# Kernel tuning notes

Hardware: AMD Instinct MI355X
Metric: run time of the kernel (lower is better)

Reference implementation:

```python
import jax, jax.numpy as jnp
import numpy as np


def setup_inputs() -> dict:
    key = jax.random.key(0)
    X = jax.random.normal(key, (8, 64, 64, 64), dtype=jnp.float32)
    return {"X": X}


def reference(X):
    N, C, h, w = X.shape
    x1 = X.reshape(N, C, h * w)            # [N, C, HW]
    x2 = jnp.transpose(x1, (0, 2, 1))      # [N, HW, C]
    scores = jnp.einsum('bnc,bcm->bnm', x2, x1)  # [N, HW, HW]
    c = jax.nn.softmax(scores, axis=2)
    out = jnp.einsum('bnm,bmc->bnc', c, x2)      # [N, HW, C]
    out = jnp.transpose(out, (0, 2, 1)).reshape(N, C, h, w)
    return out
```

## Files before the change

kernel.cpp:

```cpp
#include <hip/hip_runtime.h>
#include <math.h>


#define SEQ 4096
#define DIM 64
#define LDB 72
#define LDO 68
#define LDS2 68
#define QSCALE 1.2011224087864498f

typedef __attribute__((ext_vector_type(8)))  short short8;
typedef __attribute__((ext_vector_type(4)))  float f32x4;
typedef __attribute__((ext_vector_type(16))) float f32x16;

__device__ __forceinline__ unsigned short f2bf(float f) {
    union { float f; unsigned int u; } x; x.f = f;
    unsigned int u = x.u + 0x7FFFu + ((x.u >> 16) & 1u);
    return (unsigned short)(u >> 16);
}
__device__ __forceinline__ float bf2f(unsigned short h) {
    union { unsigned int u; float f; } x; x.u = ((unsigned int)h) << 16; return x.f;
}
__device__ __forceinline__ float fast_exp2(float x) {
#if __has_builtin(__builtin_amdgcn_exp2f)
    return __builtin_amdgcn_exp2f(x);
#else
    float r;
    asm("v_exp_f32 %0, %1\n\ts_nop 0" : "=v"(r) : "v"(x));
    return r;
#endif
}
__device__ __forceinline__ float fast_rcp(float x) {
#if __has_builtin(__builtin_amdgcn_rcpf)
    return __builtin_amdgcn_rcpf(x);
#else
    return 1.f / x;
#endif
}

__global__ __launch_bounds__(256) void prepass4(const float* __restrict__ X,
                                                unsigned short* __restrict__ Kf,
                                                unsigned short* __restrict__ Vf,
                                                float* __restrict__ Norms,
                                                float* __restrict__ MaxPart) {
    __shared__ __align__(16) unsigned short sT[64 * LDS2];
    __shared__ __align__(16) unsigned short sVu[64 * LDS2];
    __shared__ float sRed[4];
    const int b = blockIdx.y, m0 = blockIdx.x * 64;
    const float* Xb = X + (size_t)b * DIM * SEQ;
    const int t = threadIdx.x, w = t >> 6;
    const int mw = t & 15, cg = t >> 4;

    #pragma unroll
    for (int cr = 0; cr < 4; ++cr) {
        const int c = cg * 4 + cr;
        const f32x4 v = *(const f32x4*)(Xb + (size_t)c * SEQ + m0 + 4 * mw);
        *(ushort4*)(sVu + c * LDS2 + 4 * mw) =
            make_ushort4(f2bf(v.x), f2bf(v.y), f2bf(v.z), f2bf(v.w));
        sT[(4 * mw + 0) * LDS2 + c] = f2bf(v.x * QSCALE);
        sT[(4 * mw + 1) * LDS2 + c] = f2bf(v.y * QSCALE);
        sT[(4 * mw + 2) * LDS2 + c] = f2bf(v.z * QSCALE);
        sT[(4 * mw + 3) * LDS2 + c] = f2bf(v.w * QSCALE);
    }
    __syncthreads();

    {
        const int l = t & 63, ch = t >> 6;
        const int l31 = l & 31, hi = l >> 5;
        #pragma unroll
        for (int tl = 0; tl < 2; ++tl) {
            const short8 a = *(const short8*)(sT + (tl * 32 + l31) * LDS2 + ch * 16 + hi * 8);
            const size_t off = (size_t)b * 262144
                             + (size_t)(((m0 >> 5) + tl) * 4 + ch) * 512 + (size_t)l * 8;
            *(short8*)(Kf + off) = a;
        }
    }

    {
        const int m = t >> 2, ck = t & 3;
        const short8 a0 = *(const short8*)(sT + m * LDS2 + ck * 16);
        const short8 a1 = *(const short8*)(sT + m * LDS2 + ck * 16 + 8);
        float s = 0.f;
        #pragma unroll
        for (int i = 0; i < 8; ++i) {
            const float f0 = bf2f((unsigned short)a0[i]);
            const float f1 = bf2f((unsigned short)a1[i]);
            s += f0 * f0 + f1 * f1;
        }
        s += __shfl_xor(s, 1);
        s += __shfl_xor(s, 2);
        const float nm = sqrtf(s);
        if (ck == 0) Norms[(size_t)b * SEQ + m0 + m] = nm;

        float mx = nm;
        #pragma unroll
        for (int d = 4; d < 64; d <<= 1) mx = fmaxf(mx, __shfl_xor(mx, d));
        if ((t & 63) == 0) sRed[w] = mx;
    }

    {
        const int l = t & 63, pc = t >> 6;
        const int p = pc >> 1, ct = pc & 1;
        const int l31 = l & 31, hi = l >> 5;
        const int crow = (ct * 32 + l31) * LDS2;
        #pragma unroll
        for (int tl = 0; tl < 2; ++tl) {
            const int kbase = tl * 32 + p * 16 + hi * 4;
            const ushort4 g0 = *(const ushort4*)(sVu + crow + kbase);
            const ushort4 g1 = *(const ushort4*)(sVu + crow + kbase + 8);
            union { ushort4 g[2]; short8 v; } cat;
            cat.g[0] = g0; cat.g[1] = g1;
            const size_t off = (size_t)b * 262144
                             + (size_t)(((m0 >> 5) + tl) * 4 + p * 2 + ct) * 512 + (size_t)l * 8;
            *(short8*)(Vf + off) = cat.v;
        }
    }

    __syncthreads();
    if (t == 0)
        MaxPart[b * 64 + blockIdx.x] =
            fmaxf(fmaxf(sRed[0], sRed[1]), fmaxf(sRed[2], sRed[3]));
}

#if __has_builtin(__builtin_amdgcn_global_load_lds)
#define STAGE(BI, SOFF)                                                            \
    {                                                                              \
        unsigned short* dst_ = ring + (BI) * 4096 + (w ? 2048 : 0);                \
        const unsigned short* src_ = (w ? vgp : kgp) + (SOFF);                     \
        _Pragma("unroll")                                                          \
        for (int j_ = 0; j_ < 4; ++j_)                                             \
            __builtin_amdgcn_global_load_lds(                                      \
                (const __attribute__((address_space(1))) unsigned int*)(const void*)(src_ + j_ * 512), \
                (__attribute__((address_space(3))) unsigned int*)(void*)(dst_ + j_ * 512),             \
                16, 0, 0);                                                         \
    }
#else
#define STAGE(BI, SOFF)                                                            \
    {                                                                              \
        unsigned short* dst_ = ring + (BI) * 4096 + (w ? 2048 : 0) + lane * 8;     \
        const unsigned short* src_ = (w ? vgp : kgp) + (SOFF);                     \
        _Pragma("unroll")                                                          \
        for (int j_ = 0; j_ < 4; ++j_)                                             \
            *(short8*)(dst_ + j_ * 512) = *(const short8*)(src_ + j_ * 512);       \
    }
#endif

#define ATTN_STEP32(KF, VF)                                                        \
    {                                                                              \
        f32x16 aq = cin16;                                                         \
        _Pragma("unroll")                                                          \
        for (int ch_ = 0; ch_ < 4; ++ch_)                                          \
            aq = __builtin_amdgcn_mfma_f32_32x32x16_bf16(KF[ch_], qf[ch_], aq, 0, 0, 0); \
        float p_[16];                                                              \
        _Pragma("unroll")                                                          \
        for (int r_ = 0; r_ < 16; ++r_) p_[r_] = fast_exp2(aq[r_]);                \
        lp4 += (f32x4){p_[0], p_[1], p_[2], p_[3]};                                \
        lp4 += (f32x4){p_[4], p_[5], p_[6], p_[7]};                                \
        lp4 += (f32x4){p_[8], p_[9], p_[10], p_[11]};                              \
        lp4 += (f32x4){p_[12], p_[13], p_[14], p_[15]};                            \
        short8 pa_[2];                                                             \
        _Pragma("unroll")                                                          \
        for (int ph_ = 0; ph_ < 2; ++ph_) {                                        \
            union { unsigned u[4]; short8 v; } pk_;                                \
            _Pragma("unroll")                                                      \
            for (int k_ = 0; k_ < 4; ++k_)                                         \
                pk_.u[k_] = __builtin_amdgcn_perm(                                 \
                    __float_as_uint(p_[8 * ph_ + 2 * k_ + 1]),                     \
                    __float_as_uint(p_[8 * ph_ + 2 * k_]), 0x07060302u);           \
            pa_[ph_] = pk_.v;                                                      \
        }                                                                          \
        _Pragma("unroll")                                                          \
        for (int ct_ = 0; ct_ < 2; ++ct_) {                                        \
            acc_o[ct_] = __builtin_amdgcn_mfma_f32_32x32x16_bf16(                  \
                pa_[0], VF[0][ct_], acc_o[ct_], 0, 0, 0);                          \
            acc_o[ct_] = __builtin_amdgcn_mfma_f32_32x32x16_bf16(                  \
                pa_[1], VF[1][ct_], acc_o[ct_], 0, 0, 0);                          \
        }                                                                          \
    }

template <bool PARTIAL>
__global__ __launch_bounds__(128, 4) void attn_split4(const unsigned short* __restrict__ Kf,
                                                      const unsigned short* __restrict__ Vf,
                                                      const float* __restrict__ Norms,
                                                      const float* __restrict__ MaxPart,
                                                      unsigned short* __restrict__ Obf,
                                                      float* __restrict__ Lbase,
                                                      float* __restrict__ Out,
                                                      int niter) {
    __shared__ __align__(16) unsigned char smem[17408];
    unsigned short* ring = (unsigned short*)smem;
    float*          sO   = (float*)smem;

    const int tid  = threadIdx.x;
    const int lane = tid & 63;
    const int w    = tid >> 6;
    const int l31  = lane & 31;
    const int hi   = lane >> 5;

    const int gid  = blockIdx.x + 64 * (blockIdx.y + 8 * blockIdx.z);
    const int b    = gid & 7;
    const int rest = gid >> 3;
    const int s0   = (rest & 63) * 64;
    const int h    = rest >> 6;
    const int kt0  = h * niter;
    const unsigned short* Kfb = Kf + (size_t)b * 262144;
    const unsigned short* Vfb = Vf + (size_t)b * 262144;

    float mxn = MaxPart[b * 64 + lane];
    #pragma unroll
    for (int d = 1; d < 64; d <<= 1) mxn = fmaxf(mxn, __shfl_xor(mxn, d));

    short8 qf[4];
    const int qtile = (s0 >> 5) + w;
    #pragma unroll
    for (int ch = 0; ch < 4; ++ch)
        qf[ch] = *(const short8*)(Kfb + (size_t)(qtile * 4 + ch) * 512 + lane * 8);
    f32x16 cin16;
    {
        const float mrow = Norms[(size_t)b * SEQ + s0 + 32 * w + l31] * mxn;
        #pragma unroll
        for (int r = 0; r < 16; ++r) cin16[r] = -mrow;
    }

    f32x16 acc_o[2];
    #pragma unroll
    for (int ct = 0; ct < 2; ++ct)
        #pragma unroll
        for (int r = 0; r < 16; ++r) acc_o[ct][r] = 0.f;
    f32x4 lp4 = (f32x4){0.f, 0.f, 0.f, 0.f};

    const unsigned short* kgp = Kfb + lane * 8;
    const unsigned short* vgp = Vfb + lane * 8;

    STAGE(0, (size_t)kt0 * 2048);
    __syncthreads();

    for (int it = 0; it < niter; ++it) {
        const int cur = it & 1;
        if (it + 1 < niter)
            STAGE(cur ^ 1, (size_t)(kt0 + it + 1) * 2048);

        const unsigned short* Kb = ring + cur * 4096;
        const unsigned short* Vb = Kb + 2048;
        short8 kf[4], vf[2][2];
        #pragma unroll
        for (int ch = 0; ch < 4; ++ch)
            kf[ch] = *(const short8*)(Kb + ch * 512 + lane * 8);
        #pragma unroll
        for (int p = 0; p < 2; ++p)
            #pragma unroll
            for (int ct = 0; ct < 2; ++ct)
                vf[p][ct] = *(const short8*)(Vb + (p * 2 + ct) * 512 + lane * 8);

        ATTN_STEP32(kf, vf);
        __syncthreads();
    }

    float lp = (lp4[0] + lp4[1]) + (lp4[2] + lp4[3]);
    lp += __shfl_xor(lp, 32);

    if (PARTIAL) {
        if (hi == 0)
            (Lbase + (size_t)h * 8 * SEQ)[(size_t)b * SEQ + s0 + 32 * w + l31] = lp;
    } else {
        #pragma unroll
        for (int r = 0; r < 16; ++r) {
            const float inv = fast_rcp(__shfl(lp, (r & 3) + 8 * (r >> 2) + 4 * hi));
            #pragma unroll
            for (int ct = 0; ct < 2; ++ct) acc_o[ct][r] *= inv;
        }
    }

    __syncthreads();
    #pragma unroll
    for (int ct = 0; ct < 2; ++ct) {
        const int c = ct * 32 + l31;
        #pragma unroll
        for (int r = 0; r < 16; ++r)
            sO[c * LDO + 32 * w + (r & 3) + 8 * (r >> 2) + 4 * hi] = acc_o[ct][r];
    }
    __syncthreads();
    const int mw = tid & 15, cg = tid >> 4;
    if (PARTIAL) {
        unsigned short* Op = Obf + (size_t)h * 8 * DIM * SEQ;
        #pragma unroll
        for (int cc = 0; cc < 8; ++cc) {
            const int c = cg + 8 * cc;
            const f32x4 v = *(const f32x4*)(sO + c * LDO + 4 * mw);
            *(ushort4*)(Op + ((size_t)b * DIM + c) * SEQ + s0 + 4 * mw) =
                make_ushort4(f2bf(v.x), f2bf(v.y), f2bf(v.z), f2bf(v.w));
        }
    } else {
        #pragma unroll
        for (int cc = 0; cc < 8; ++cc) {
            const int c = cg + 8 * cc;
            const f32x4 v = *(const f32x4*)(sO + c * LDO + 4 * mw);
            *(f32x4*)(Out + ((size_t)b * DIM + c) * SEQ + s0 + 4 * mw) = v;
        }
    }
}

__global__ __launch_bounds__(256) void combine4(const unsigned short* __restrict__ Obf,
                                                const float* __restrict__ Lp,
                                                float* __restrict__ Out) {
    const int gid = blockIdx.x * 256 + threadIdx.x;
    const size_t base = (size_t)gid * 4;
    const int s = (int)(base & 4095);
    const int b = (int)(base >> 18);
    f32x4 os = (f32x4){0.f, 0.f, 0.f, 0.f};
    f32x4 ls = (f32x4){0.f, 0.f, 0.f, 0.f};
    #pragma unroll
    for (int h = 0; h < 4; ++h) {
        const ushort4 o = *(const ushort4*)(Obf + (size_t)h * 2097152 + base);
        os[0] += bf2f(o.x); os[1] += bf2f(o.y); os[2] += bf2f(o.z); os[3] += bf2f(o.w);
        const f32x4 l = *(const f32x4*)(Lp + (size_t)h * 8 * SEQ + b * SEQ + s);
        #pragma unroll
        for (int i = 0; i < 4; ++i) ls[i] += l[i];
    }
    f32x4 o;
    #pragma unroll
    for (int i = 0; i < 4; ++i) o[i] = os[i] / ls[i];
    *(f32x4*)(Out + base) = o;
}

__global__ __launch_bounds__(256, 2) void attn_fallback(const float* __restrict__ X,
                                                        float* __restrict__ Out) {
    __shared__ __align__(16) unsigned char smem[27648];
    unsigned short* sK = (unsigned short*)smem;
    unsigned short* sV = (unsigned short*)(smem + 9216);
    unsigned short* sP = (unsigned short*)(smem + 18432);
    float*          sO = (float*)smem;
    const int tid  = threadIdx.x;
    const int lane = tid & 63;
    const int w    = tid >> 6;
    const int l15  = lane & 15;
    const int quad = lane >> 4;
    const int b  = blockIdx.y;
    const int s0 = blockIdx.x * 64;
    const float* Xb = X + (size_t)b * DIM * SEQ;
    const int mgrp = tid & 15;
    const int c0   = tid >> 4;

    for (int cc = 0; cc < 4; ++cc) {
        int c = c0 + 16 * cc;
        const f32x4 v = *(const f32x4*)(Xb + (size_t)c * SEQ + s0 + 4 * mgrp);
        sK[(4 * mgrp + 0) * LDB + c] = f2bf(v.x);
        sK[(4 * mgrp + 1) * LDB + c] = f2bf(v.y);
        sK[(4 * mgrp + 2) * LDB + c] = f2bf(v.z);
        sK[(4 * mgrp + 3) * LDB + c] = f2bf(v.w);
    }
    __syncthreads();
    short8 qf0, qf1;
    {
        const int row = 16 * w + l15;
        qf0 = *(const short8*)(sK + row * LDB + quad * 8);
        qf1 = *(const short8*)(sK + row * LDB + 32 + quad * 8);
    }
    __syncthreads();
    f32x4 acc_o[4];
    for (int ct = 0; ct < 4; ++ct) acc_o[ct] = (f32x4){0.f, 0.f, 0.f, 0.f};
    float m_i[4] = {-1e30f, -1e30f, -1e30f, -1e30f};
    float l_i[4] = {0.f, 0.f, 0.f, 0.f};
    for (int kt = 0; kt < SEQ / 64; ++kt) {
        const int m0 = kt * 64;
        for (int cc = 0; cc < 4; ++cc) {
            int c = c0 + 16 * cc;
            const f32x4 v = *(const f32x4*)(Xb + (size_t)c * SEQ + m0 + 4 * mgrp);
            unsigned short h0 = f2bf(v.x), h1 = f2bf(v.y), h2 = f2bf(v.z), h3 = f2bf(v.w);
            *(ushort4*)(sV + c * LDB + 4 * mgrp) = make_ushort4(h0, h1, h2, h3);
            sK[(4 * mgrp + 0) * LDB + c] = h0;
            sK[(4 * mgrp + 1) * LDB + c] = h1;
            sK[(4 * mgrp + 2) * LDB + c] = h2;
            sK[(4 * mgrp + 3) * LDB + c] = h3;
        }
        __syncthreads();
        short8 vf[2][4];
        for (int ks = 0; ks < 2; ++ks)
            for (int ct = 0; ct < 4; ++ct)
                vf[ks][ct] = *(const short8*)(sV + (16 * ct + l15) * LDB + ks * 32 + quad * 8);
        f32x4 acc_s[4];
        for (int mt = 0; mt < 4; ++mt) {
            const int row = 16 * mt + l15;
            const short8 kf0 = *(const short8*)(sK + row * LDB + quad * 8);
            const short8 kf1 = *(const short8*)(sK + row * LDB + 32 + quad * 8);
            f32x4 a = (f32x4){0.f, 0.f, 0.f, 0.f};
            a = __builtin_amdgcn_mfma_f32_16x16x32_bf16(qf0, kf0, a, 0, 0, 0);
            a = __builtin_amdgcn_mfma_f32_16x16x32_bf16(qf1, kf1, a, 0, 0, 0);
            acc_s[mt] = a;
        }
        float alpha[4];
        for (int r = 0; r < 4; ++r) {
            float mx = fmaxf(fmaxf(acc_s[0][r], acc_s[1][r]), fmaxf(acc_s[2][r], acc_s[3][r]));
            mx = fmaxf(mx, __shfl_xor(mx, 1));
            mx = fmaxf(mx, __shfl_xor(mx, 2));
            mx = fmaxf(mx, __shfl_xor(mx, 4));
            mx = fmaxf(mx, __shfl_xor(mx, 8));
            const float mnew = fmaxf(m_i[r], mx);
            alpha[r] = __expf(m_i[r] - mnew);
            m_i[r] = mnew;
        }
        float rowsum[4] = {0.f, 0.f, 0.f, 0.f};
        unsigned short pb[4][4];
        for (int mt = 0; mt < 4; ++mt)
            for (int r = 0; r < 4; ++r) {
                const float p = __expf(acc_s[mt][r] - m_i[r]);
                rowsum[r] += p;
                pb[mt][r] = f2bf(p);
            }
        for (int r = 0; r < 4; ++r) {
            float s = rowsum[r];
            s += __shfl_xor(s, 1);
            s += __shfl_xor(s, 2);
            s += __shfl_xor(s, 4);
            s += __shfl_xor(s, 8);
            l_i[r] = alpha[r] * l_i[r] + s;
        }
        for (int ct = 0; ct < 4; ++ct)
            for (int r = 0; r < 4; ++r)
                acc_o[ct][r] *= alpha[r];
        for (int mt = 0; mt < 4; ++mt)
            for (int r = 0; r < 4; ++r)
                sP[(16 * w + quad * 4 + r) * LDB + l15 + 16 * mt] = pb[mt][r];
        __syncthreads();
        const short8 pf0 = *(const short8*)(sP + (16 * w + l15) * LDB + quad * 8);
        const short8 pf1 = *(const short8*)(sP + (16 * w + l15) * LDB + 32 + quad * 8);
        for (int ct = 0; ct < 4; ++ct) {
            acc_o[ct] = __builtin_amdgcn_mfma_f32_16x16x32_bf16(pf0, vf[0][ct], acc_o[ct], 0, 0, 0);
            acc_o[ct] = __builtin_amdgcn_mfma_f32_16x16x32_bf16(pf1, vf[1][ct], acc_o[ct], 0, 0, 0);
        }
    }
    float inv[4];
    for (int r = 0; r < 4; ++r) inv[r] = 1.f / l_i[r];
    for (int ct = 0; ct < 4; ++ct) {
        const int c = 16 * ct + l15;
        for (int r = 0; r < 4; ++r)
            sO[c * LDO + 16 * w + quad * 4 + r] = acc_o[ct][r] * inv[r];
    }
    __syncthreads();
    for (int cc = 0; cc < 4; ++cc) {
        const int c = c0 + 16 * cc;
        const f32x4 v = *(const f32x4*)(sO + c * LDO + 4 * mgrp);
        *(f32x4*)(Out + (size_t)b * DIM * SEQ + (size_t)c * SEQ + s0 + 4 * mgrp) = v;
    }
}

extern "C" void kernel_launch(void* const* d_in, const int* in_sizes, int n_in,
                              void* d_out, int out_size, void* d_ws, size_t ws_size,
                              hipStream_t stream) {
    const float* X = (const float*)d_in[0];
    float* Out = (float*)d_out;
    const size_t elems = (size_t)8 * SEQ * DIM;
    const size_t offVf    = elems * 2;
    const size_t offNorms = offVf + elems * 2;
    const size_t offMaxP  = offNorms + (size_t)8 * SEQ * 4;
    const size_t offObf   = offMaxP + 8 * 64 * 4;
    const size_t offLp    = offObf + 4 * elems * 2;
    const size_t need     = offLp + 4 * (size_t)8 * SEQ * 4;

    if (ws_size >= need) {
        unsigned short* Kf = (unsigned short*)d_ws;
        unsigned short* Vf = (unsigned short*)((char*)d_ws + offVf);
        float* Norms   = (float*)((char*)d_ws + offNorms);
        float* MaxPart = (float*)((char*)d_ws + offMaxP);
        unsigned short* Obf = (unsigned short*)((char*)d_ws + offObf);
        float* Lp = (float*)((char*)d_ws + offLp);
        prepass4<<<dim3(64, 8), 256, 0, stream>>>(X, Kf, Vf, Norms, MaxPart);
        attn_split4<true><<<dim3(64, 8, 4), 128, 0, stream>>>(Kf, Vf, Norms, MaxPart,
                                                              Obf, Lp, nullptr, 32);
        combine4<<<(int)(elems / 1024), 256, 0, stream>>>(Obf, Lp, Out);
    } else {
        attn_fallback<<<dim3(64, 8), 256, 0, stream>>>(X, Out);
    }
}
```

Before: 110.5 us.

## Deepen K/V ring to four slots and process two tiles per iteration

Grows the LDS ring from two to four 32-row tile slots. Each loop iteration now loads two tiles into registers, prefetches the next two, and processes both before a single barrier, which halves the barrier count and gives the loads more time to overlap. The QK^T MFMA chain is split into two independent accumulators that are summed before the exp, shortening the dependent MFMA chain. Launch bounds drop from 4 to 2 blocks per CU to allow more registers. The new loop assumes niter is even and costs occupancy and extra LDS.

```diff
diff --git a/kernel.cpp b/kernel.cpp
--- a/kernel.cpp
+++ b/kernel.cpp
@@ -123,10 +123,10 @@
 }
 
 #if __has_builtin(__builtin_amdgcn_global_load_lds)
-#define STAGE(BI, SOFF)                                                            \
+#define STAGE(SLOT, TIDX)                                                          \
     {                                                                              \
-        unsigned short* dst_ = ring + (BI) * 4096 + (w ? 2048 : 0);                \
-        const unsigned short* src_ = (w ? vgp : kgp) + (SOFF);                     \
+        unsigned short* dst_ = ring + (SLOT) * 4096 + (w ? 2048 : 0);              \
+        const unsigned short* src_ = (w ? vgp : kgp) + (size_t)(TIDX) * 2048;      \
         _Pragma("unroll")                                                          \
         for (int j_ = 0; j_ < 4; ++j_)                                             \
             __builtin_amdgcn_global_load_lds(                                      \
@@ -135,25 +135,43 @@
                 16, 0, 0);                                                         \
     }
 #else
-#define STAGE(BI, SOFF)                                                            \
+#define STAGE(SLOT, TIDX)                                                          \
     {                                                                              \
-        unsigned short* dst_ = ring + (BI) * 4096 + (w ? 2048 : 0) + lane * 8;     \
-        const unsigned short* src_ = (w ? vgp : kgp) + (SOFF);                     \
+        unsigned short* dst_ = ring + (SLOT) * 4096 + (w ? 2048 : 0) + lane * 8;   \
+        const unsigned short* src_ = (w ? vgp : kgp) + (size_t)(TIDX) * 2048;      \
         _Pragma("unroll")                                                          \
         for (int j_ = 0; j_ < 4; ++j_)                                             \
             *(short8*)(dst_ + j_ * 512) = *(const short8*)(src_ + j_ * 512);       \
     }
 #endif
 
+#define LOADT(KF, VF, S)                                                           \
+    {                                                                              \
+        const unsigned short* Kb_ = ring + (S) * 4096;                             \
+        const unsigned short* Vb_ = Kb_ + 2048;                                    \
+        _Pragma("unroll")                                                          \
+        for (int ch_ = 0; ch_ < 4; ++ch_)                                          \
+            KF[ch_] = *(const short8*)(Kb_ + ch_ * 512 + lane * 8);                \
+        _Pragma("unroll")                                                          \
+        for (int p_ = 0; p_ < 2; ++p_)                                             \
+            _Pragma("unroll")                                                      \
+            for (int ct_ = 0; ct_ < 2; ++ct_)                                      \
+                VF[p_][ct_] = *(const short8*)(Vb_ + (p_ * 2 + ct_) * 512 + lane * 8); \
+    }
+
 #define ATTN_STEP32(KF, VF)                                                        \
     {                                                                              \
-        f32x16 aq = cin16;                                                         \
-        _Pragma("unroll")                                                          \
-        for (int ch_ = 0; ch_ < 4; ++ch_)                                          \
-            aq = __builtin_amdgcn_mfma_f32_32x32x16_bf16(KF[ch_], qf[ch_], aq, 0, 0, 0); \
+        f32x16 aqA = cin16;                                                        \
+        f32x16 aqB;                                                                \
+        _Pragma("unroll")                                                          \
+        for (int r_ = 0; r_ < 16; ++r_) aqB[r_] = 0.f;                             \
+        aqA = __builtin_amdgcn_mfma_f32_32x32x16_bf16(KF[0], qf[0], aqA, 0, 0, 0); \
+        aqB = __builtin_amdgcn_mfma_f32_32x32x16_bf16(KF[2], qf[2], aqB, 0, 0, 0); \
+        aqA = __builtin_amdgcn_mfma_f32_32x32x16_bf16(KF[1], qf[1], aqA, 0, 0, 0); \
+        aqB = __builtin_amdgcn_mfma_f32_32x32x16_bf16(KF[3], qf[3], aqB, 0, 0, 0); \
         float p_[16];                                                              \
         _Pragma("unroll")                                                          \
-        for (int r_ = 0; r_ < 16; ++r_) p_[r_] = fast_exp2(aq[r_]);                \
+        for (int r_ = 0; r_ < 16; ++r_) p_[r_] = fast_exp2(aqA[r_] + aqB[r_]);     \
         lp4 += (f32x4){p_[0], p_[1], p_[2], p_[3]};                                \
         lp4 += (f32x4){p_[4], p_[5], p_[6], p_[7]};                                \
         lp4 += (f32x4){p_[8], p_[9], p_[10], p_[11]};                              \
@@ -179,7 +197,7 @@
     }
 
 template <bool PARTIAL>
-__global__ __launch_bounds__(128, 4) void attn_split4(const unsigned short* __restrict__ Kf,
+__global__ __launch_bounds__(128, 2) void attn_split4(const unsigned short* __restrict__ Kf,
                                                       const unsigned short* __restrict__ Vf,
                                                       const float* __restrict__ Norms,
                                                       const float* __restrict__ MaxPart,
@@ -187,7 +205,7 @@
                                                       float* __restrict__ Lbase,
                                                       float* __restrict__ Out,
                                                       int niter) {
-    __shared__ __align__(16) unsigned char smem[17408];
+    __shared__ __align__(16) unsigned char smem[32768];
     unsigned short* ring = (unsigned short*)smem;
     float*          sO   = (float*)smem;
 
@@ -232,27 +250,19 @@
     const unsigned short* kgp = Kfb + lane * 8;
     const unsigned short* vgp = Vfb + lane * 8;
 
-    STAGE(0, (size_t)kt0 * 2048);
-    __syncthreads();
-
-    for (int it = 0; it < niter; ++it) {
-        const int cur = it & 1;
-        if (it + 1 < niter)
-            STAGE(cur ^ 1, (size_t)(kt0 + it + 1) * 2048);
-
-        const unsigned short* Kb = ring + cur * 4096;
-        const unsigned short* Vb = Kb + 2048;
-        short8 kf[4], vf[2][2];
-        #pragma unroll
-        for (int ch = 0; ch < 4; ++ch)
-            kf[ch] = *(const short8*)(Kb + ch * 512 + lane * 8);
-        #pragma unroll
-        for (int p = 0; p < 2; ++p)
-            #pragma unroll
-            for (int ct = 0; ct < 2; ++ct)
-                vf[p][ct] = *(const short8*)(Vb + (p * 2 + ct) * 512 + lane * 8);
-
-        ATTN_STEP32(kf, vf);
+    STAGE(0, kt0);
+    STAGE(1, kt0 + 1);
+    __syncthreads();
+
+    for (int t = 0; t < niter; t += 2) {
+        const int sA = t & 3, sB = (t + 1) & 3;
+        short8 kfA[4], vfA[2][2], kfB[4], vfB[2][2];
+        LOADT(kfA, vfA, sA);
+        LOADT(kfB, vfB, sB);
+        if (t + 2 < niter) STAGE((t + 2) & 3, kt0 + t + 2);
+        if (t + 3 < niter) STAGE((t + 3) & 3, kt0 + t + 3);
+        ATTN_STEP32(kfA, vfA);
+        ATTN_STEP32(kfB, vfB);
         __syncthreads();
     }
 
```

Result: slower. 119.6 us (+8.2%).
